# Optimization experiments

Hardware: AMD Instinct MI355X
Metric: run time of the kernel (lower is better)

The kernel has to match this reference:

```python
import jax, jax.numpy as jnp
import numpy as np

IN = 4096   # input_size * 2 (is_bichar)
H = 2048    # hidden_size
C = 4096    # number of lexicon inputs


def setup_inputs() -> dict:
    key = jax.random.key(0)
    ks = jax.random.split(key, 12)
    s = 0.02
    return {
        "x": jax.random.normal(ks[0], (1, IN), jnp.float32),
        "c_input": jax.random.normal(ks[1], (C, H), jnp.float32),
        "h0": jax.random.normal(ks[2], (1, H), jnp.float32),
        "c0": jax.random.normal(ks[3], (1, H), jnp.float32),
        "W_ih": jax.random.normal(ks[4], (4 * H, IN), jnp.float32) * s,
        "b_ih": jnp.zeros((4 * H,), jnp.float32),
        "W_hh": jax.random.normal(ks[5], (4 * H, H), jnp.float32) * s,
        "b_hh": jnp.zeros((4 * H,), jnp.float32),
        "aW_ih": jax.random.normal(ks[6], (H, IN), jnp.float32) * s,
        "ab_ih": jnp.zeros((H,), jnp.float32),
        "aW_hh": jax.random.normal(ks[7], (H, H), jnp.float32) * s,
        "ab_hh": jnp.zeros((H,), jnp.float32),
    }


def reference(x, c_input, h0, c0, W_ih, b_ih, W_hh, b_hh, aW_ih, ab_ih, aW_hh, ab_hh):
    # gate pre-activations: [1, 4H]
    lstm_vec = x @ W_ih.T + b_ih + h0 @ W_hh.T + b_hh
    i, f, o, g = jnp.split(lstm_vec, 4, axis=1)
    i = jax.nn.sigmoid(i)
    f = jax.nn.sigmoid(f + 1.0)  # computed but unused when lexicon is non-empty (faithful)
    g = jnp.tanh(g)
    o = jax.nn.sigmoid(o)
    # alpha over lexicon entries: [C, H] (x-projection broadcasts over C)
    alpha = jax.nn.sigmoid(x @ aW_ih.T + ab_ih + c_input @ aW_hh.T + ab_hh)
    # exp-normalize over the (C+1) candidates per hidden unit
    w = jnp.exp(jnp.concatenate([i, alpha], axis=0))  # [C+1, H]
    w = w / w.sum(axis=0)
    merge = jnp.concatenate([g, c_input], axis=0)  # [C+1, H]
    c1 = (merge * w).sum(axis=0, keepdims=True)  # [1, H]
    h1 = o * jnp.tanh(c1)
    return h1, c1
```

## Files before the change

kernel.cpp:

```cpp
#include <hip/hip_runtime.h>
#include <hip/hip_bf16.h>
#include <cstdint>

#define HDIM 2048
#define INDIM 4096
#define CDIM 4096
#define KDIM 2048

typedef __attribute__((ext_vector_type(4))) int int4v;

__device__ __forceinline__ void gload16(const void* g, void* l) {
  __builtin_amdgcn_global_load_lds(
      (const __attribute__((address_space(1))) void*)g,
      (__attribute__((address_space(3))) void*)l, 16, 0, 0);
}

__global__ __launch_bounds__(256) void k_quant_xa2(
    const float* __restrict__ c_input, const float* __restrict__ aW_hh,
    int8_t* __restrict__ a8, int8_t* __restrict__ b8,
    float* __restrict__ dAs, float* __restrict__ dBs,
    const float* __restrict__ x,
    const float* __restrict__ aW_ih, const float* __restrict__ ab_ih,
    const float* __restrict__ ab_hh,
    float* __restrict__ xa2, float* __restrict__ accz) {
  const int t = threadIdx.x;
  const int wid = t >> 6, lane = t & 63;

  if (blockIdx.x < 1536) {
    if (blockIdx.x == 0) {
#pragma unroll
      for (int i = 0; i < 16; ++i) accz[i * 256 + t] = 0.f;
    }
    const int row = blockIdx.x * 4 + wid;
    const float* src; int8_t* dst; float* dsc; int r;
    if (row < CDIM) { src = c_input; dst = a8; dsc = dAs; r = row; }
    else            { src = aW_hh;  dst = b8; dsc = dBs; r = row - CDIM; }
    const float4* s4 = (const float4*)(src + (size_t)r * KDIM);
    float4 v[8];
#pragma unroll
    for (int it = 0; it < 8; ++it) v[it] = s4[it * 64 + lane];
    float am = 0.f;
#pragma unroll
    for (int it = 0; it < 8; ++it)
      am = fmaxf(am, fmaxf(fmaxf(fabsf(v[it].x), fabsf(v[it].y)),
                           fmaxf(fabsf(v[it].z), fabsf(v[it].w))));
#pragma unroll
    for (int off = 32; off > 0; off >>= 1) am = fmaxf(am, __shfl_xor(am, off));
    am = fmaxf(am, 1e-20f);
    const float inv = 127.0f / am;
    uint32_t* qd = (uint32_t*)(dst + (size_t)r * KDIM);
#pragma unroll
    for (int it = 0; it < 8; ++it) {
      uint32_t p = (uint32_t)(__float2int_rn(v[it].x * inv) & 0xFF)
                 | ((uint32_t)(__float2int_rn(v[it].y * inv) & 0xFF) << 8)
                 | ((uint32_t)(__float2int_rn(v[it].z * inv) & 0xFF) << 16)
                 | ((uint32_t)(__float2int_rn(v[it].w * inv) & 0xFF) << 24);
      qd[it * 64 + lane] = p;
    }
    if (lane == 0) dsc[r] = am * (1.0f / 127.0f);
    return;
  }

  const int h = (blockIdx.x - 1536) * 4 + wid;
  const float4* x4 = (const float4*)x;
  const float4* wr4 = (const float4*)(aW_ih + (size_t)h * INDIM);
  float sum = 0.f;
#pragma unroll
  for (int g = 0; g < 2; ++g) {
    float4 w[8];
#pragma unroll
    for (int it = 0; it < 8; ++it) w[it] = wr4[(g * 8 + it) * 64 + lane];
#pragma unroll
    for (int it = 0; it < 8; ++it) {
      float4 xv = x4[(g * 8 + it) * 64 + lane];
      sum += w[it].x * xv.x + w[it].y * xv.y + w[it].z * xv.z + w[it].w * xv.w;
    }
  }
#pragma unroll
  for (int off = 32; off > 0; off >>= 1) sum += __shfl_down(sum, off);
  if (lane == 0) xa2[h] = sum + ab_ih[h] + ab_hh[h];
}

__global__ __launch_bounds__(256, 4) void k_gemm_gemv(
    const int8_t* __restrict__ A, const int8_t* __restrict__ B,
    const float* __restrict__ dAs, const float* __restrict__ dBs,
    const float* __restrict__ c_in, const float* __restrict__ xa2,
    float* __restrict__ acc_se, float* __restrict__ acc_sce,
    const float* __restrict__ x, const float* __restrict__ h0,
    const float* __restrict__ W_ih, const float* __restrict__ b_ih,
    const float* __restrict__ W_hh, const float* __restrict__ b_hh,
    float* __restrict__ i_sig, float* __restrict__ o_sig,
    float* __restrict__ g_tanh) {
  __shared__ uint8_t As[2][8192];
  __shared__ uint8_t Bs[2][8192];
  const int t = threadIdx.x;
  const int lane = t & 63, wid = t >> 6;

  if (blockIdx.x < 512) {
    const int wr = wid >> 1, wc = wid & 1;
    const int l15 = lane & 15, l4 = lane >> 4;
    const int bm = blockIdx.x & 31, bn = blockIdx.x >> 5;
    const int m0 = bm * 128, n0 = bn * 128;

    int4v acc[4][4] = {};

    const int trow = t >> 2;
    const int tcol = ((t & 3) * 16) ^ ((trow & 3) << 4);
    const int8_t* Arow = A + (size_t)(m0 + trow) * KDIM + tcol;
    const int8_t* Brow = B + (size_t)(n0 + trow) * KDIM + tcol;

#define STAGE(buf, k0)                                                          \
    do {                                                                        \
      _Pragma("unroll")                                                         \
      for (int qq = 0; qq < 2; ++qq) {                                          \
        gload16(Arow + (size_t)qq * 64 * KDIM + (k0), As[buf] + qq * 4096 + t * 16); \
        gload16(Brow + (size_t)qq * 64 * KDIM + (k0), Bs[buf] + qq * 4096 + t * 16); \
      }                                                                         \
    } while (0)

    STAGE(0, 0);
    __syncthreads();

    int cur = 0;
    for (int ti = 0; ti < KDIM / 64; ++ti) {
      if (ti < KDIM / 64 - 1) STAGE(cur ^ 1, (ti + 1) * 64);
      int4v af[4], bfr[4];
#pragma unroll
      for (int m = 0; m < 4; ++m) {
        const int r = wr * 64 + m * 16 + l15;
        af[m] = *(const int4v*)(As[cur] + r * 64 + ((l4 * 16) ^ ((r & 3) << 4)));
      }
#pragma unroll
      for (int n = 0; n < 4; ++n) {
        const int r = wc * 64 + n * 16 + l15;
        bfr[n] = *(const int4v*)(Bs[cur] + r * 64 + ((l4 * 16) ^ ((r & 3) << 4)));
      }
#pragma unroll
      for (int m = 0; m < 4; ++m)
#pragma unroll
        for (int n = 0; n < 4; ++n)
          acc[m][n] = __builtin_amdgcn_mfma_i32_16x16x64_i8(af[m], bfr[n], acc[m][n], 0, 0, 0);
      __syncthreads();
      cur ^= 1;
    }
#undef STAGE

#pragma unroll
    for (int n = 0; n < 4; ++n) {
      const int hcol = n0 + wc * 64 + n * 16 + l15;
      const float xa = xa2[hcol];
      const float db = dBs[hcol];
      float se = 0.f, sce = 0.f;
#pragma unroll
      for (int m = 0; m < 4; ++m) {
        const int jbase = m0 + wr * 64 + m * 16 + l4 * 4;
#pragma unroll
        for (int rr = 0; rr < 4; ++rr) {
          const float sc = dAs[jbase + rr] * db;
          float z = (float)acc[m][n][rr] * sc + xa;
          float s = 1.f / (1.f + __expf(-z));
          float e = __expf(s);
          se += e;
          sce += c_in[(size_t)(jbase + rr) * HDIM + hcol] * e;
        }
      }
      se += __shfl_xor(se, 16); se += __shfl_xor(se, 32);
      sce += __shfl_xor(sce, 16); sce += __shfl_xor(sce, 32);
      if (l4 == 0) {
        atomicAdd(&acc_se[hcol], se);
        atomicAdd(&acc_sce[hcol], sce);
      }
    }
    return;
  }

  const int vr = (blockIdx.x - 512) * 4 + wid;
  const int typ = vr >> 11;
  const int h = vr & (HDIM - 1);
  const int grow = (typ == 0) ? h : (typ == 1) ? (2 * HDIM + h) : (3 * HDIM + h);
  float sum = 0.f;
  const float4* x4 = (const float4*)x;
  const float4* wr4 = (const float4*)(W_ih + (size_t)grow * INDIM);
#pragma unroll
  for (int g = 0; g < 2; ++g) {
    float4 w[8];
#pragma unroll
    for (int it = 0; it < 8; ++it) w[it] = wr4[(g * 8 + it) * 64 + lane];
#pragma unroll
    for (int it = 0; it < 8; ++it) {
      float4 xv = x4[(g * 8 + it) * 64 + lane];
      sum += w[it].x * xv.x + w[it].y * xv.y + w[it].z * xv.z + w[it].w * xv.w;
    }
  }
  {
    const float4* wh4 = (const float4*)(W_hh + (size_t)grow * HDIM);
    const float4* h4 = (const float4*)h0;
    float4 w[8];
#pragma unroll
    for (int it = 0; it < 8; ++it) w[it] = wh4[it * 64 + lane];
#pragma unroll
    for (int it = 0; it < 8; ++it) {
      float4 hv = h4[it * 64 + lane];
      sum += w[it].x * hv.x + w[it].y * hv.y + w[it].z * hv.z + w[it].w * hv.w;
    }
  }
#pragma unroll
  for (int off = 32; off > 0; off >>= 1) sum += __shfl_down(sum, off);
  if (lane == 0) {
    float z = sum + b_ih[grow] + b_hh[grow];
    if (typ == 0)      i_sig[h] = 1.f / (1.f + expf(-z));
    else if (typ == 1) o_sig[h] = 1.f / (1.f + expf(-z));
    else               g_tanh[h] = tanhf(z);
  }
}

__global__ __launch_bounds__(256) void k_final(
    const float* __restrict__ i_sig, const float* __restrict__ o_sig,
    const float* __restrict__ g_tanh, const float* __restrict__ acc_se,
    const float* __restrict__ acc_sce, float* __restrict__ out) {
  int h = blockIdx.x * 256 + threadIdx.x;
  if (h >= HDIM) return;
  float wi = expf(i_sig[h]);
  float tot = acc_se[h] + wi;
  float c1 = (acc_sce[h] + g_tanh[h] * wi) / tot;
  float h1 = o_sig[h] * tanhf(c1);
  out[h] = h1;
  out[HDIM + h] = c1;
}

extern "C" void kernel_launch(void* const* d_in, const int* in_sizes, int n_in,
                              void* d_out, int out_size, void* d_ws, size_t ws_size,
                              hipStream_t stream) {
  const float* x     = (const float*)d_in[0];
  const float* c_inp = (const float*)d_in[1];
  const float* h0    = (const float*)d_in[2];
  const float* W_ih  = (const float*)d_in[4];
  const float* b_ih  = (const float*)d_in[5];
  const float* W_hh  = (const float*)d_in[6];
  const float* b_hh  = (const float*)d_in[7];
  const float* aW_ih = (const float*)d_in[8];
  const float* ab_ih = (const float*)d_in[9];
  const float* aW_hh = (const float*)d_in[10];
  const float* ab_hh = (const float*)d_in[11];
  float* out = (float*)d_out;

  char* ws = (char*)d_ws;
  int8_t* a8 = (int8_t*)ws;
  int8_t* b8 = a8 + (size_t)CDIM * KDIM;
  float* dAs = (float*)(b8 + (size_t)HDIM * KDIM);
  float* dBs = dAs + CDIM;
  float* fb  = dBs + HDIM;
  float* i_sig   = fb;
  float* o_sig   = fb + HDIM;
  float* g_tanh  = fb + 2 * HDIM;
  float* xa2     = fb + 3 * HDIM;
  float* acc_se  = fb + 4 * HDIM;
  float* acc_sce = fb + 5 * HDIM;

  k_quant_xa2<<<2048, 256, 0, stream>>>(
      c_inp, aW_hh, a8, b8, dAs, dBs, x, aW_ih, ab_ih, ab_hh, xa2, acc_se);
  k_gemm_gemv<<<512 + 1536, 256, 0, stream>>>(
      a8, b8, dAs, dBs, c_inp, xa2, acc_se, acc_sce,
      x, h0, W_ih, b_ih, W_hh, b_hh, i_sig, o_sig, g_tanh);
  k_final<<<(HDIM + 255) / 256, 256, 0, stream>>>(i_sig, o_sig, g_tanh,
                                                  acc_se, acc_sce, out);
}
```

Baseline: 65.64 us.

## Co-schedule GEMM and GEMV waves in one block with per-wave async pipelines

```diff
diff --git a/kernel.cpp b/kernel.cpp
--- a/kernel.cpp
+++ b/kernel.cpp
@@ -81,7 +81,7 @@
   if (lane == 0) xa2[h] = sum + ab_ih[h] + ab_hh[h];
 }
 
-__global__ __launch_bounds__(256, 4) void k_gemm_gemv(
+__global__ __launch_bounds__(512, 4) void k_fat(
     const int8_t* __restrict__ A, const int8_t* __restrict__ B,
     const float* __restrict__ dAs, const float* __restrict__ dBs,
     const float* __restrict__ c_in, const float* __restrict__ xa2,
@@ -91,69 +91,78 @@
     const float* __restrict__ W_hh, const float* __restrict__ b_hh,
     float* __restrict__ i_sig, float* __restrict__ o_sig,
     float* __restrict__ g_tanh) {
-  __shared__ uint8_t As[2][8192];
-  __shared__ uint8_t Bs[2][8192];
+  __shared__ uint8_t lds[4][2][2][4096];
   const int t = threadIdx.x;
-  const int lane = t & 63, wid = t >> 6;
-
-  if (blockIdx.x < 512) {
+  const int wid = t >> 6, lane = t & 63;
+
+  if (wid < 4) {
     const int wr = wid >> 1, wc = wid & 1;
     const int l15 = lane & 15, l4 = lane >> 4;
     const int bm = blockIdx.x & 31, bn = blockIdx.x >> 5;
-    const int m0 = bm * 128, n0 = bn * 128;
+    const int arow0 = bm * 128 + wr * 64;
+    const int brow0 = bn * 128 + wc * 64;
+    uint8_t* wbase = &lds[wid][0][0][0];
+
+    const int srow = lane >> 2;
+    const int scolb = ((lane & 3) * 16) ^ ((srow & 3) << 4);
+    const int8_t* Asrc = A + (size_t)(arow0 + srow) * KDIM + scolb;
+    const int8_t* Bsrc = B + (size_t)(brow0 + srow) * KDIM + scolb;
 
     int4v acc[4][4] = {};
 
-    const int trow = t >> 2;
-    const int tcol = ((t & 3) * 16) ^ ((trow & 3) << 4);
-    const int8_t* Arow = A + (size_t)(m0 + trow) * KDIM + tcol;
-    const int8_t* Brow = B + (size_t)(n0 + trow) * KDIM + tcol;
-
-#define STAGE(buf, k0)                                                          \
-    do {                                                                        \
-      _Pragma("unroll")                                                         \
-      for (int qq = 0; qq < 2; ++qq) {                                          \
-        gload16(Arow + (size_t)qq * 64 * KDIM + (k0), As[buf] + qq * 4096 + t * 16); \
-        gload16(Brow + (size_t)qq * 64 * KDIM + (k0), Bs[buf] + qq * 4096 + t * 16); \
-      }                                                                         \
+#define STG(buf, kt)                                                           \
+    do {                                                                       \
+      _Pragma("unroll")                                                        \
+      for (int q = 0; q < 4; ++q) {                                            \
+        gload16(Asrc + (size_t)q * 16 * KDIM + (size_t)(kt) * 64,              \
+                wbase + (buf) * 8192 + q * 1024 + lane * 16);                  \
+        gload16(Bsrc + (size_t)q * 16 * KDIM + (size_t)(kt) * 64,              \
+                wbase + (buf) * 8192 + 4096 + q * 1024 + lane * 16);           \
+      }                                                                        \
     } while (0)
 
-    STAGE(0, 0);
-    __syncthreads();
-
-    int cur = 0;
+    STG(0, 0);
+    STG(1, 1);
+
     for (int ti = 0; ti < KDIM / 64; ++ti) {
-      if (ti < KDIM / 64 - 1) STAGE(cur ^ 1, (ti + 1) * 64);
-      int4v af[4], bfr[4];
+      const int cur = ti & 1;
+      if (ti < KDIM / 64 - 1) {
+        asm volatile("s_waitcnt vmcnt(8)" ::: "memory");
+      } else {
+        asm volatile("s_waitcnt vmcnt(0)" ::: "memory");
+      }
+      const uint8_t* Ab = wbase + cur * 8192;
+      const uint8_t* Bb = Ab + 4096;
+      int4v bf[4];
+#pragma unroll
+      for (int n = 0; n < 4; ++n) {
+        const int r = n * 16 + l15;
+        bf[n] = *(const int4v*)(Bb + r * 64 + ((l4 * 16) ^ ((r & 3) << 4)));
+      }
 #pragma unroll
       for (int m = 0; m < 4; ++m) {
-        const int r = wr * 64 + m * 16 + l15;
-        af[m] = *(const int4v*)(As[cur] + r * 64 + ((l4 * 16) ^ ((r & 3) << 4)));
-      }
-#pragma unroll
-      for (int n = 0; n < 4; ++n) {
-        const int r = wc * 64 + n * 16 + l15;
-        bfr[n] = *(const int4v*)(Bs[cur] + r * 64 + ((l4 * 16) ^ ((r & 3) << 4)));
-      }
-#pragma unroll
-      for (int m = 0; m < 4; ++m)
+        const int r = m * 16 + l15;
+        int4v af = *(const int4v*)(Ab + r * 64 + ((l4 * 16) ^ ((r & 3) << 4)));
 #pragma unroll
         for (int n = 0; n < 4; ++n)
-          acc[m][n] = __builtin_amdgcn_mfma_i32_16x16x64_i8(af[m], bfr[n], acc[m][n], 0, 0, 0);
-      __syncthreads();
-      cur ^= 1;
-    }
-#undef STAGE
+          acc[m][n] = __builtin_amdgcn_mfma_i32_16x16x64_i8(af, bf[n], acc[m][n], 0, 0, 0);
+      }
+      if (ti < KDIM / 64 - 2) {
+        asm volatile("s_waitcnt lgkmcnt(0)" ::: "memory");
+        STG(cur, ti + 2);
+      }
+    }
+#undef STG
 
 #pragma unroll
     for (int n = 0; n < 4; ++n) {
-      const int hcol = n0 + wc * 64 + n * 16 + l15;
+      const int hcol = brow0 + n * 16 + l15;
       const float xa = xa2[hcol];
       const float db = dBs[hcol];
       float se = 0.f, sce = 0.f;
 #pragma unroll
       for (int m = 0; m < 4; ++m) {
-        const int jbase = m0 + wr * 64 + m * 16 + l4 * 4;
+        const int jbase = arow0 + m * 16 + l4 * 4;
 #pragma unroll
         for (int rr = 0; rr < 4; ++rr) {
           const float sc = dAs[jbase + rr] * db;
@@ -174,43 +183,44 @@
     return;
   }
 
-  const int vr = (blockIdx.x - 512) * 4 + wid;
-  const int typ = vr >> 11;
-  const int h = vr & (HDIM - 1);
-  const int grow = (typ == 0) ? h : (typ == 1) ? (2 * HDIM + h) : (3 * HDIM + h);
-  float sum = 0.f;
+  const int g = blockIdx.x * 4 + (wid - 4);
   const float4* x4 = (const float4*)x;
-  const float4* wr4 = (const float4*)(W_ih + (size_t)grow * INDIM);
-#pragma unroll
-  for (int g = 0; g < 2; ++g) {
-    float4 w[8];
-#pragma unroll
-    for (int it = 0; it < 8; ++it) w[it] = wr4[(g * 8 + it) * 64 + lane];
-#pragma unroll
-    for (int it = 0; it < 8; ++it) {
-      float4 xv = x4[(g * 8 + it) * 64 + lane];
-      sum += w[it].x * xv.x + w[it].y * xv.y + w[it].z * xv.z + w[it].w * xv.w;
-    }
-  }
-  {
-    const float4* wh4 = (const float4*)(W_hh + (size_t)grow * HDIM);
-    const float4* h4 = (const float4*)h0;
-    float4 w[8];
-#pragma unroll
-    for (int it = 0; it < 8; ++it) w[it] = wh4[it * 64 + lane];
-#pragma unroll
-    for (int it = 0; it < 8; ++it) {
-      float4 hv = h4[it * 64 + lane];
-      sum += w[it].x * hv.x + w[it].y * hv.y + w[it].z * hv.z + w[it].w * hv.w;
-    }
-  }
-#pragma unroll
-  for (int off = 32; off > 0; off >>= 1) sum += __shfl_down(sum, off);
-  if (lane == 0) {
-    float z = sum + b_ih[grow] + b_hh[grow];
-    if (typ == 0)      i_sig[h] = 1.f / (1.f + expf(-z));
-    else if (typ == 1) o_sig[h] = 1.f / (1.f + expf(-z));
-    else               g_tanh[h] = tanhf(z);
+  const float4* h4 = (const float4*)h0;
+#pragma unroll
+  for (int typ = 0; typ < 3; ++typ) {
+    const int grow = (typ == 0) ? g : (typ == 1) ? (2 * HDIM + g) : (3 * HDIM + g);
+    float sum = 0.f;
+    const float4* wr4 = (const float4*)(W_ih + (size_t)grow * INDIM);
+#pragma unroll
+    for (int gg = 0; gg < 2; ++gg) {
+      float4 w[8];
+#pragma unroll
+      for (int it = 0; it < 8; ++it) w[it] = wr4[(gg * 8 + it) * 64 + lane];
+#pragma unroll
+      for (int it = 0; it < 8; ++it) {
+        float4 xv = x4[(gg * 8 + it) * 64 + lane];
+        sum += w[it].x * xv.x + w[it].y * xv.y + w[it].z * xv.z + w[it].w * xv.w;
+      }
+    }
+    {
+      const float4* wh4 = (const float4*)(W_hh + (size_t)grow * HDIM);
+      float4 w[8];
+#pragma unroll
+      for (int it = 0; it < 8; ++it) w[it] = wh4[it * 64 + lane];
+#pragma unroll
+      for (int it = 0; it < 8; ++it) {
+        float4 hv = h4[it * 64 + lane];
+        sum += w[it].x * hv.x + w[it].y * hv.y + w[it].z * hv.z + w[it].w * hv.w;
+      }
+    }
+#pragma unroll
+    for (int off = 32; off > 0; off >>= 1) sum += __shfl_down(sum, off);
+    if (lane == 0) {
+      float z = sum + b_ih[grow] + b_hh[grow];
+      if (typ == 0)      i_sig[g] = 1.f / (1.f + expf(-z));
+      else if (typ == 1) o_sig[g] = 1.f / (1.f + expf(-z));
+      else               g_tanh[g] = tanhf(z);
+    }
   }
 }
 
@@ -259,7 +269,7 @@
 
   k_quant_xa2<<<2048, 256, 0, stream>>>(
       c_inp, aW_hh, a8, b8, dAs, dBs, x, aW_ih, ab_ih, ab_hh, xa2, acc_se);
-  k_gemm_gemv<<<512 + 1536, 256, 0, stream>>>(
+  k_fat<<<512, 512, 0, stream>>>(
       a8, b8, dAs, dBs, c_inp, xa2, acc_se, acc_sce,
       x, h0, W_ih, b_ih, W_hh, b_hh, i_sig, o_sig, g_tanh);
   k_final<<<(HDIM + 255) / 256, 256, 0, stream>>>(i_sig, o_sig, g_tanh,
```

After: 87.10 us. 1.33x slower.
